# Optimization experiments

Measured on AMD Instinct MI355X. Metric: run time of the kernel, lower is better.

The kernel has to match this reference:

```python
import jax, jax.numpy as jnp
import numpy as np

B, N, D = 8, 2048, 1024

def setup_inputs() -> dict:
    key = jax.random.key(0)
    ks = jax.random.split(key, 7)
    s = 1.0 / np.sqrt(D)
    return {
        "x": jax.random.normal(ks[0], (B, N, D), dtype=jnp.float32),
        "Wq": jax.random.uniform(ks[1], (D, D), jnp.float32, -s, s),
        "bq": jax.random.uniform(ks[2], (D,), jnp.float32, -s, s),
        "Wk": jax.random.uniform(ks[3], (D, D), jnp.float32, -s, s),
        "bk": jax.random.uniform(ks[4], (D,), jnp.float32, -s, s),
        "Wv": jax.random.uniform(ks[5], (D, D), jnp.float32, -s, s),
        "bv": jax.random.uniform(ks[6], (D,), jnp.float32, -s, s),
    }

def reference(x, Wq, bq, Wk, bk, Wv, bv):
    # torch nn.Linear: y = x @ W.T + b
    q = jnp.einsum('bnd,ed->bne', x, Wq) + bq
    k = jnp.einsum('bnd,ed->bne', x, Wk) + bk
    v = jnp.einsum('bnd,ed->bne', x, Wv) + bv
    # NOTE: original applies NO 1/sqrt(d) scaling
    scores = jnp.einsum('bnd,bmd->bnm', q, k)  # [B, N, N]
    probs = jax.nn.softmax(scores, axis=-1)
    return jnp.einsum('bnm,bmd->bnd', probs, v)
```

## Files before the change

kernel.cpp:

```cpp
#include <hip/hip_runtime.h>


typedef _Float16 f16;
typedef _Float16 f16x4 __attribute__((ext_vector_type(4)));
typedef _Float16 f16x8 __attribute__((ext_vector_type(8)));
typedef float f32x4 __attribute__((ext_vector_type(4)));

#define Nn_ 2048
#define Dd 1024

typedef const __attribute__((address_space(1))) void gvoid;
typedef __attribute__((address_space(3))) void lvoid;

__device__ __forceinline__ void glds16(const void* g, void* l) {
    __builtin_amdgcn_global_load_lds((gvoid*)g, (lvoid*)l, 16, 0, 0);
}
#define BARRIER()  asm volatile("s_barrier" ::: "memory")
#define LGKM0()    asm volatile("s_waitcnt lgkmcnt(0)" ::: "memory")
#define VM6()      asm volatile("s_waitcnt vmcnt(6)" ::: "memory")
#define VM0()      asm volatile("s_waitcnt vmcnt(0)" ::: "memory")
#define PRIO1()    __builtin_amdgcn_s_setprio(1)
#define PRIO0()    __builtin_amdgcn_s_setprio(0)
#define MFMA(a, b, c) __builtin_amdgcn_mfma_f32_16x16x32_f16((a), (b), (c), 0, 0, 0)

__global__ void cvt_kernel(const float4* __restrict__ in, f16x4* __restrict__ out, int n4) {
    int i = blockIdx.x * 256 + threadIdx.x;
    if (i >= n4) return;
    float4 f = in[i];
    f16x4 h;
    h.x = (_Float16)f.x; h.y = (_Float16)f.y; h.z = (_Float16)f.z; h.w = (_Float16)f.w;
    out[i] = h;
}

__global__ void concat_bias(const float* __restrict__ bq, const float* __restrict__ bk,
                            const float* __restrict__ bv, float* __restrict__ o) {
    int i = blockIdx.x * 256 + threadIdx.x;
    if (i >= 3072) return;
    o[i] = (i < 1024) ? bq[i] : (i < 2048 ? bk[i - 1024] : bv[i - 2048]);
}

__global__ __launch_bounds__(512) void gemm_bt(
    const f16* __restrict__ A, const f16* __restrict__ Bm,
    const float* __restrict__ bias, void* __restrict__ Cout,
    f16* __restrict__ qh, f16* __restrict__ kh, f16* __restrict__ vT,
    int K, int lda, int ldb, int ldc, int mode,
    long aStride, long bStride, long cStride)
{
    __shared__ f16 sm[65536];
    const int tid = threadIdx.x;
    const int lane = tid & 63, wid = tid >> 6;
    const int quad = lane >> 4, l16 = lane & 15;
    const int wm = wid & 1;
    const int wn = wid >> 1;
    const long m0 = (long)blockIdx.x * 256, n0 = (long)blockIdx.y * 256;
    A += (long)blockIdx.z * aStride;
    Bm += (long)blockIdx.z * bStride;

    const int lr = tid >> 3;
    const int sc8 = ((tid & 7) ^ (lr & 7)) * 8;
    const f16* pa = A + (m0 + lr) * (long)lda + sc8;
    const f16* pb = Bm + (n0 + lr) * (long)ldb + sc8;
    const long a64 = 64L * lda, b64 = 64L * ldb;

    const int aRow = (wm * 128 + l16) * 64;
    const int bRow = (wn * 64 + l16) * 64;
    const int co0 = (quad ^ (l16 & 7)) * 8;
    const int co1 = ((quad + 4) ^ (l16 & 7)) * 8;

    f32x4 acc[8][4];
#pragma unroll
    for (int i = 0; i < 8; i++)
#pragma unroll
        for (int j = 0; j < 4; j++) acc[i][j] = 0.0f;

    const int nk = K >> 6;

#pragma unroll
    for (int q = 0; q < 4; ++q) glds16(pa + q * a64, sm + tid * 8 + q * 4096);
#pragma unroll
    for (int q = 0; q < 4; ++q) glds16(pb + q * b64, sm + 16384 + tid * 8 + q * 4096);
    if (nk > 1) {
#pragma unroll
        for (int q = 0; q < 4; ++q)
            glds16(pa + q * a64 + 64, sm + 32768 + tid * 8 + q * 4096);
#pragma unroll
        for (int q = 0; q < 4; ++q)
            glds16(pb + q * b64 + 64, sm + 49152 + tid * 8 + q * 4096);
        VM6();
    } else {
        VM0();
    }
    BARRIER();

    f16x8 af0[2][4], af1[2][4], bf0[2][2], bf1[2][2];
    {
        const f16* As = sm;
        const f16* Bs = sm + 16384;
#pragma unroll
        for (int i = 0; i < 4; ++i) {
            af0[0][i] = *(const f16x8*)(As + aRow + i * 1024 + co0);
            af0[1][i] = *(const f16x8*)(As + aRow + i * 1024 + co1);
        }
#pragma unroll
        for (int j = 0; j < 2; ++j) {
            bf0[0][j] = *(const f16x8*)(Bs + bRow + j * 1024 + co0);
            bf0[1][j] = *(const f16x8*)(Bs + bRow + j * 1024 + co1);
        }
    }
    LGKM0();

    int bo = 0;
    for (int t = 0; t < nk; ++t) {
        const f16* As = sm + bo;
        const f16* Bs = As + 16384;
        const f16* An = sm + (bo ^ 32768);
        const f16* Bn = An + 16384;
        const long kt2 = (long)(t + 2) * 64;
        const bool st = (t + 2) < nk;

        BARRIER();
#pragma unroll
        for (int j = 0; j < 2; ++j) {
            bf1[0][j] = *(const f16x8*)(Bs + bRow + 2048 + j * 1024 + co0);
            bf1[1][j] = *(const f16x8*)(Bs + bRow + 2048 + j * 1024 + co1);
        }
        if (st) {
            glds16(pa + 0 * a64 + kt2, sm + bo + tid * 8);
            glds16(pa + 2 * a64 + kt2, sm + bo + tid * 8 + 2 * 4096);
        }
        PRIO1();
#pragma unroll
        for (int i = 0; i < 4; ++i)
#pragma unroll
            for (int j = 0; j < 2; ++j) {
                acc[i][j] = MFMA(af0[0][i], bf0[0][j], acc[i][j]);
                acc[i][j] = MFMA(af0[1][i], bf0[1][j], acc[i][j]);
            }
        PRIO0(); LGKM0();

        BARRIER();
#pragma unroll
        for (int i = 0; i < 4; ++i) {
            af1[0][i] = *(const f16x8*)(As + aRow + 4096 + i * 1024 + co0);
            af1[1][i] = *(const f16x8*)(As + aRow + 4096 + i * 1024 + co1);
        }
        if (st) {
            glds16(pb + 0 * b64 + kt2, sm + bo + 16384 + tid * 8);
            glds16(pb + 1 * b64 + kt2, sm + bo + 16384 + tid * 8 + 4096);
        }
        PRIO1();
#pragma unroll
        for (int i = 0; i < 4; ++i)
#pragma unroll
            for (int j = 0; j < 2; ++j) {
                acc[i][2 + j] = MFMA(af0[0][i], bf1[0][j], acc[i][2 + j]);
                acc[i][2 + j] = MFMA(af0[1][i], bf1[1][j], acc[i][2 + j]);
            }
        PRIO0(); LGKM0();

        BARRIER();
        if (st) {
            glds16(pb + 2 * b64 + kt2, sm + bo + 16384 + tid * 8 + 2 * 4096);
            glds16(pb + 3 * b64 + kt2, sm + bo + 16384 + tid * 8 + 3 * 4096);
        }
        PRIO1();
#pragma unroll
        for (int i = 0; i < 4; ++i)
#pragma unroll
            for (int j = 0; j < 2; ++j) {
                acc[4 + i][j] = MFMA(af1[0][i], bf0[0][j], acc[4 + i][j]);
                acc[4 + i][j] = MFMA(af1[1][i], bf0[1][j], acc[4 + i][j]);
            }
        PRIO0();
        if (st) { VM6(); } else { VM0(); }

        BARRIER();
        if (t + 1 < nk) {
#pragma unroll
            for (int i = 0; i < 4; ++i) {
                af0[0][i] = *(const f16x8*)(An + aRow + i * 1024 + co0);
                af0[1][i] = *(const f16x8*)(An + aRow + i * 1024 + co1);
            }
#pragma unroll
            for (int j = 0; j < 2; ++j) {
                bf0[0][j] = *(const f16x8*)(Bn + bRow + j * 1024 + co0);
                bf0[1][j] = *(const f16x8*)(Bn + bRow + j * 1024 + co1);
            }
        }
        if (st) {
            glds16(pa + 1 * a64 + kt2, sm + bo + tid * 8 + 4096);
            glds16(pa + 3 * a64 + kt2, sm + bo + tid * 8 + 3 * 4096);
        }
        PRIO1();
#pragma unroll
        for (int i = 0; i < 4; ++i)
#pragma unroll
            for (int j = 0; j < 2; ++j) {
                acc[4 + i][2 + j] = MFMA(af1[0][i], bf1[0][j], acc[4 + i][2 + j]);
                acc[4 + i][2 + j] = MFMA(af1[1][i], bf1[1][j], acc[4 + i][2 + j]);
            }
        PRIO0(); LGKM0();
        bo ^= 32768;
    }

    if (mode == 2) {
        float* O = (float*)Cout + (long)blockIdx.z * cStride;
#pragma unroll
        for (int ct = 0; ct < 4; ct++) {
            long n = n0 + wn * 64 + ct * 16 + l16;
#pragma unroll
            for (int rt = 0; rt < 8; rt++) {
                long mb = m0 + wm * 128 + rt * 16 + quad * 4;
#pragma unroll
                for (int r = 0; r < 4; r++)
                    O[(mb + r) * ldc + n] = acc[rt][ct][r];
            }
        }
    } else {
        if (blockIdx.y < 8) {
            f16* O = (blockIdx.y < 4) ? qh : kh;
#pragma unroll
            for (int ct = 0; ct < 4; ct++) {
                long n = n0 + wn * 64 + ct * 16 + l16;
                float bs = bias[n];
                long n1 = n & 1023;
#pragma unroll
                for (int rt = 0; rt < 8; rt++) {
                    long mb = m0 + wm * 128 + rt * 16 + quad * 4;
#pragma unroll
                    for (int r = 0; r < 4; r++)
                        O[(mb + r) * 1024 + n1] = (f16)(acc[rt][ct][r] + bs);
                }
            }
        } else {
            const long nb = n0 - 2048;
            const long vbase = (m0 >> 11) * (long)(Dd * Nn_) + (m0 & 2047);
#pragma unroll
            for (int g = 0; g < 4; ++g) {
                __syncthreads();
                if (wn == g) {
#pragma unroll
                    for (int ct = 0; ct < 4; ++ct) {
                        int cl = ct * 16 + l16;
                        float bs = bias[n0 + g * 64 + cl];
#pragma unroll
                        for (int rt = 0; rt < 8; rt++) {
                            int row = wm * 128 + rt * 16 + quad * 4;
#pragma unroll
                            for (int r = 0; r < 4; r++)
                                sm[cl * 264 + row + r] = (f16)(acc[rt][ct][r] + bs);
                        }
                    }
                }
                __syncthreads();
                const int rowi = tid >> 3, c = (tid & 7) * 32;
                f16* dst = vT + vbase + (nb + g * 64 + rowi) * (long)Nn_ + c;
                const f16* src = sm + rowi * 264 + c;
                *(f16x8*)(dst) = *(const f16x8*)(src);
                *(f16x8*)(dst + 8) = *(const f16x8*)(src + 8);
                *(f16x8*)(dst + 16) = *(const f16x8*)(src + 16);
                *(f16x8*)(dst + 24) = *(const f16x8*)(src + 24);
            }
        }
    }
}

__global__ __launch_bounds__(256) void softmax_rows(float* __restrict__ S) {
    const int row = blockIdx.x * 4 + (threadIdx.x >> 6);
    const int lane = threadIdx.x & 63;
    float* Sr = S + (long)row * 2048;
    const float4* R4 = (const float4*)Sr;
    float4 t[8];
#pragma unroll
    for (int i = 0; i < 8; i++) t[i] = R4[lane + 64 * i];
    float mx = -1e30f;
#pragma unroll
    for (int i = 0; i < 8; i++)
        mx = fmaxf(mx, fmaxf(fmaxf(t[i].x, t[i].y), fmaxf(t[i].z, t[i].w)));
#pragma unroll
    for (int off = 1; off < 64; off <<= 1) mx = fmaxf(mx, __shfl_xor(mx, off, 64));
    float se = 0.0f;
#pragma unroll
    for (int i = 0; i < 8; i++) {
        t[i].x = __expf(t[i].x - mx); t[i].y = __expf(t[i].y - mx);
        t[i].z = __expf(t[i].z - mx); t[i].w = __expf(t[i].w - mx);
        se += t[i].x + t[i].y + t[i].z + t[i].w;
    }
#pragma unroll
    for (int off = 1; off < 64; off <<= 1) se += __shfl_xor(se, off, 64);
    const float li = 1.0f / se;
    f16x4* P4 = (f16x4*)Sr;
#pragma unroll
    for (int i = 0; i < 8; i++) {
        f16x4 h;
        h.x = (_Float16)(t[i].x * li); h.y = (_Float16)(t[i].y * li);
        h.z = (_Float16)(t[i].z * li); h.w = (_Float16)(t[i].w * li);
        P4[lane + 64 * i] = h;
    }
}

extern "C" void kernel_launch(void* const* d_in, const int* in_sizes, int n_in,
                              void* d_out, int out_size, void* d_ws, size_t ws_size,
                              hipStream_t stream) {
    const float* x  = (const float*)d_in[0];
    const float* Wq = (const float*)d_in[1];
    const float* bq = (const float*)d_in[2];
    const float* Wk = (const float*)d_in[3];
    const float* bk = (const float*)d_in[4];
    const float* Wv = (const float*)d_in[5];
    const float* bv = (const float*)d_in[6];

    f16* wsh = (f16*)d_ws;
    dim3 blk(512);
    const bool full = ws_size >= 234881024ULL;

    if (full) {
        f16* qh  = wsh;
        f16* kh  = wsh + 16777216;
        f16* vT  = wsh + 33554432;
        float* S = (float*)(wsh + 50331648);
        f16* xh  = wsh + 50331648;
        f16* Wh  = wsh + 67108864;
        float* bqkv = (float*)(wsh + 70254592);

        cvt_kernel<<<16384, 256, 0, stream>>>((const float4*)x, (f16x4*)xh, 4194304);
        cvt_kernel<<<1024, 256, 0, stream>>>((const float4*)Wq, (f16x4*)Wh, 262144);
        cvt_kernel<<<1024, 256, 0, stream>>>((const float4*)Wk, (f16x4*)(Wh + 1048576), 262144);
        cvt_kernel<<<1024, 256, 0, stream>>>((const float4*)Wv, (f16x4*)(Wh + 2097152), 262144);
        concat_bias<<<12, 256, 0, stream>>>(bq, bk, bv, bqkv);

        gemm_bt<<<dim3(64, 12, 1), blk, 0, stream>>>(
            xh, Wh, bqkv, nullptr, qh, kh, vT,
            1024, 1024, 1024, 0, 3, 0, 0, 0);
        gemm_bt<<<dim3(8, 8, 8), blk, 0, stream>>>(
            qh, kh, nullptr, S, nullptr, nullptr, nullptr,
            1024, 1024, 1024, 2048, 2,
            (long)Nn_ * Dd, (long)Nn_ * Dd, (long)Nn_ * Nn_);
        softmax_rows<<<4096, 256, 0, stream>>>(S);
        gemm_bt<<<dim3(8, 4, 8), blk, 0, stream>>>(
            (const f16*)S, vT, nullptr, d_out, nullptr, nullptr, nullptr,
            2048, 4096, 2048, 1024, 2,
            (long)Nn_ * 4096, (long)Dd * Nn_, (long)Nn_ * Dd);
    } else {
        f16* xh  = wsh;
        f16* Wh  = wsh + 16777216;
        float* bqkv = (float*)(wsh + 19922944);
        f16* qh  = wsh + 19929088;
        f16* kh  = qh + 16777216;
        f16* vT  = kh + 16777216;
        float* S = (float*)(vT + 16777216);

        cvt_kernel<<<16384, 256, 0, stream>>>((const float4*)x, (f16x4*)xh, 4194304);
        cvt_kernel<<<1024, 256, 0, stream>>>((const float4*)Wq, (f16x4*)Wh, 262144);
        cvt_kernel<<<1024, 256, 0, stream>>>((const float4*)Wk, (f16x4*)(Wh + 1048576), 262144);
        cvt_kernel<<<1024, 256, 0, stream>>>((const float4*)Wv, (f16x4*)(Wh + 2097152), 262144);
        concat_bias<<<12, 256, 0, stream>>>(bq, bk, bv, bqkv);

        gemm_bt<<<dim3(64, 12, 1), blk, 0, stream>>>(
            xh, Wh, bqkv, nullptr, qh, kh, vT,
            1024, 1024, 1024, 0, 3, 0, 0, 0);

        for (int h = 0; h < 2; ++h) {
            const long b0 = 4L * h;
            gemm_bt<<<dim3(8, 8, 4), blk, 0, stream>>>(
                qh + b0 * Nn_ * Dd, kh + b0 * Nn_ * Dd, nullptr, S,
                nullptr, nullptr, nullptr,
                1024, 1024, 1024, 2048, 2,
                (long)Nn_ * Dd, (long)Nn_ * Dd, (long)Nn_ * Nn_);
            softmax_rows<<<2048, 256, 0, stream>>>(S);
            gemm_bt<<<dim3(8, 4, 4), blk, 0, stream>>>(
                (const f16*)S, vT + b0 * Dd * Nn_, nullptr,
                (float*)d_out + b0 * Nn_ * Dd, nullptr, nullptr, nullptr,
                2048, 4096, 2048, 1024, 2,
                (long)Nn_ * 4096, (long)Dd * Nn_, (long)Nn_ * Dd);
        }
    }
}
```

Before: 435.3 us.

## Add 128x256-tile triple-buffered GEMM for the QK^T score computation

Adds a new gemm128 kernel with 128x256 output tiles, a K-step of 32 and a three-stage LDS ring fed by global_load_lds, and uses it for the Q·K^T score GEMM instead of the 256x256 kernel. The grid doubles from 512 to 1024 blocks, which should improve CU occupancy and wave balance on the 256-CU device, and the deeper prefetch is meant to hide load latency. In exchange, each tile reloads more operand data per output, and the fp32 score stores are scalar per element, which may cost bandwidth.

New measurement: 454.0 us. +4.3%, slower.

```diff
diff --git a/kernel.cpp b/kernel.cpp
--- a/kernel.cpp
+++ b/kernel.cpp
@@ -23,6 +23,13 @@
 #define PRIO0()    __builtin_amdgcn_s_setprio(0)
 #define MFMA(a, b, c) __builtin_amdgcn_mfma_f32_16x16x32_f16((a), (b), (c), 0, 0, 0)
 
+__device__ __forceinline__ void bar_vm3() {
+    asm volatile("s_waitcnt vmcnt(3)\n\ts_barrier" ::: "memory");
+}
+__device__ __forceinline__ void bar_vm0() {
+    asm volatile("s_waitcnt vmcnt(0)\n\ts_barrier" ::: "memory");
+}
+
 __global__ void cvt_kernel(const float4* __restrict__ in, f16x4* __restrict__ out, int n4) {
     int i = blockIdx.x * 256 + threadIdx.x;
     if (i >= n4) return;
@@ -39,7 +46,94 @@
     o[i] = (i < 1024) ? bq[i] : (i < 2048 ? bk[i - 1024] : bv[i - 2048]);
 }
 
-__global__ __launch_bounds__(512) void gemm_bt(
+__global__ __launch_bounds__(512) void gemm128(
+    const f16* __restrict__ A, const f16* __restrict__ Bm,
+    float* __restrict__ Cout,
+    int K, int lda, int ldb, int ldc,
+    long aStride, long bStride, long cStride)
+{
+    __shared__ f16 sm[36864];
+    const int tid = threadIdx.x;
+    const int lane = tid & 63, wid = tid >> 6;
+    const int quad = lane >> 4, l16 = lane & 15;
+    const int wm = (wid & 1) * 64;
+    const int wn = (wid >> 1) * 64;
+    const long m0 = (long)blockIdx.x * 128, n0 = (long)blockIdx.y * 256;
+    const int bz = blockIdx.z;
+    A += (long)bz * aStride;
+    Bm += (long)bz * bStride;
+
+    const int la = tid, lb0 = tid, lb1 = tid + 512;
+    const long arow = m0 + (la >> 2);
+    const long brow0 = n0 + (lb0 >> 2), brow1 = n0 + (lb1 >> 2);
+    const int colA  = ((la & 3) ^ ((la >> 3) & 3)) * 8;
+    const int colB0 = ((lb0 & 3) ^ ((lb0 >> 3) & 3)) * 8;
+    const int colB1 = ((lb1 & 3) ^ ((lb1 >> 3) & 3)) * 8;
+
+    const f16* pa  = A + arow * lda + colA;
+    const f16* pb0 = Bm + brow0 * ldb + colB0;
+    const f16* pb1 = Bm + brow1 * ldb + colB1;
+
+    const int fo = (quad ^ ((l16 >> 1) & 3)) * 8;
+
+    f32x4 acc[4][4];
+#pragma unroll
+    for (int i = 0; i < 4; i++)
+#pragma unroll
+        for (int j = 0; j < 4; j++) acc[i][j] = 0.0f;
+
+    const int nk = K >> 5;
+    glds16(pa, sm + la * 8);
+    glds16(pb0, sm + 4096 + lb0 * 8);
+    glds16(pb1, sm + 4096 + lb1 * 8);
+    if (nk > 1) {
+        glds16(pa + 32, sm + 12288 + la * 8);
+        glds16(pb0 + 32, sm + 16384 + lb0 * 8);
+        glds16(pb1 + 32, sm + 16384 + lb1 * 8);
+    }
+
+    int cur = 0;
+    for (int it = 0; it < nk; ++it) {
+        if (it + 1 < nk) bar_vm3(); else bar_vm0();
+        if (it + 2 < nk) {
+            f16* dst = sm + ((cur >= 1) ? (cur - 1) : 2) * 12288;
+            const int ko = (it + 2) * 32;
+            glds16(pa + ko, dst + la * 8);
+            glds16(pb0 + ko, dst + 4096 + lb0 * 8);
+            glds16(pb1 + ko, dst + 4096 + lb1 * 8);
+        }
+        const f16* As = sm + cur * 12288;
+        const f16* Bs = As + 4096;
+        f16x8 af[4], bf[4];
+#pragma unroll
+        for (int rt = 0; rt < 4; rt++)
+            af[rt] = *(const f16x8*)(As + (wm + rt * 16 + l16) * 32 + fo);
+#pragma unroll
+        for (int ct = 0; ct < 4; ct++)
+            bf[ct] = *(const f16x8*)(Bs + (wn + ct * 16 + l16) * 32 + fo);
+#pragma unroll
+        for (int rt = 0; rt < 4; rt++)
+#pragma unroll
+            for (int ct = 0; ct < 4; ct++)
+                acc[rt][ct] = MFMA(af[rt], bf[ct], acc[rt][ct]);
+        cur = (cur == 2) ? 0 : cur + 1;
+    }
+
+    float* O = Cout + (long)bz * cStride;
+#pragma unroll
+    for (int ct = 0; ct < 4; ct++) {
+        long n = n0 + wn + ct * 16 + l16;
+#pragma unroll
+        for (int rt = 0; rt < 4; rt++) {
+            long mb = m0 + wm + rt * 16 + quad * 4;
+#pragma unroll
+            for (int r = 0; r < 4; r++)
+                O[(mb + r) * ldc + n] = acc[rt][ct][r];
+        }
+    }
+}
+
+__global__ __launch_bounds__(512) void gemm256(
     const f16* __restrict__ A, const f16* __restrict__ Bm,
     const float* __restrict__ bias, void* __restrict__ Cout,
     f16* __restrict__ qh, f16* __restrict__ kh, f16* __restrict__ vT,
@@ -329,15 +423,15 @@
         cvt_kernel<<<1024, 256, 0, stream>>>((const float4*)Wv, (f16x4*)(Wh + 2097152), 262144);
         concat_bias<<<12, 256, 0, stream>>>(bq, bk, bv, bqkv);
 
-        gemm_bt<<<dim3(64, 12, 1), blk, 0, stream>>>(
+        gemm256<<<dim3(64, 12, 1), blk, 0, stream>>>(
             xh, Wh, bqkv, nullptr, qh, kh, vT,
             1024, 1024, 1024, 0, 3, 0, 0, 0);
-        gemm_bt<<<dim3(8, 8, 8), blk, 0, stream>>>(
-            qh, kh, nullptr, S, nullptr, nullptr, nullptr,
-            1024, 1024, 1024, 2048, 2,
+        gemm128<<<dim3(16, 8, 8), blk, 0, stream>>>(
+            qh, kh, S,
+            1024, 1024, 1024, 2048,
             (long)Nn_ * Dd, (long)Nn_ * Dd, (long)Nn_ * Nn_);
         softmax_rows<<<4096, 256, 0, stream>>>(S);
-        gemm_bt<<<dim3(8, 4, 8), blk, 0, stream>>>(
+        gemm256<<<dim3(8, 4, 8), blk, 0, stream>>>(
             (const f16*)S, vT, nullptr, d_out, nullptr, nullptr, nullptr,
             2048, 4096, 2048, 1024, 2,
             (long)Nn_ * 4096, (long)Dd * Nn_, (long)Nn_ * Dd);
@@ -356,19 +450,18 @@
         cvt_kernel<<<1024, 256, 0, stream>>>((const float4*)Wv, (f16x4*)(Wh + 2097152), 262144);
         concat_bias<<<12, 256, 0, stream>>>(bq, bk, bv, bqkv);
 
-        gemm_bt<<<dim3(64, 12, 1), blk, 0, stream>>>(
+        gemm256<<<dim3(64, 12, 1), blk, 0, stream>>>(
             xh, Wh, bqkv, nullptr, qh, kh, vT,
             1024, 1024, 1024, 0, 3, 0, 0, 0);
 
         for (int h = 0; h < 2; ++h) {
             const long b0 = 4L * h;
-            gemm_bt<<<dim3(8, 8, 4), blk, 0, stream>>>(
-                qh + b0 * Nn_ * Dd, kh + b0 * Nn_ * Dd, nullptr, S,
-                nullptr, nullptr, nullptr,
-                1024, 1024, 1024, 2048, 2,
+            gemm128<<<dim3(16, 8, 4), blk, 0, stream>>>(
+                qh + b0 * Nn_ * Dd, kh + b0 * Nn_ * Dd, S,
+                1024, 1024, 1024, 2048,
                 (long)Nn_ * Dd, (long)Nn_ * Dd, (long)Nn_ * Nn_);
             softmax_rows<<<2048, 256, 0, stream>>>(S);
-            gemm_bt<<<dim3(8, 4, 4), blk, 0, stream>>>(
+            gemm256<<<dim3(8, 4, 4), blk, 0, stream>>>(
                 (const f16*)S, vT + b0 * Dd * Nn_, nullptr,
                 (float*)d_out + b0 * Nn_ * Dd, nullptr, nullptr, nullptr,
                 2048, 4096, 2048, 1024, 2,
```
